# Kernel optimization log

Measured on AMD Instinct MI355X. Metric: run time of the kernel, lower is better.

Reference implementation:

```python
import jax, jax.numpy as jnp
import numpy as np

D_MODEL = 1024
N_HEADS = 16
D_K = D_MODEL // N_HEADS
B, L = 2, 2048


def setup_inputs() -> dict:
    key = jax.random.key(0)
    ks = jax.random.split(key, 11)
    s = 1.0 / np.sqrt(D_MODEL)
    return {
        "q": jax.random.normal(ks[0], (B, L, D_MODEL), jnp.float32),
        "k": jax.random.normal(ks[1], (B, L, D_MODEL), jnp.float32),
        "v": jax.random.normal(ks[2], (B, L, D_MODEL), jnp.float32),
        "w_q": jax.random.normal(ks[3], (D_MODEL, D_MODEL), jnp.float32) * s,
        "b_q": jnp.zeros((D_MODEL,), jnp.float32),
        "w_k": jax.random.normal(ks[4], (D_MODEL, D_MODEL), jnp.float32) * s,
        "b_k": jnp.zeros((D_MODEL,), jnp.float32),
        "w_v": jax.random.normal(ks[5], (D_MODEL, D_MODEL), jnp.float32) * s,
        "b_v": jnp.zeros((D_MODEL,), jnp.float32),
        "w_o": jax.random.normal(ks[6], (D_MODEL, D_MODEL), jnp.float32) * s,
        "b_o": jnp.zeros((D_MODEL,), jnp.float32),
    }


def reference(q, k, v, w_q, b_q, w_k, b_k, w_v, b_v, w_o, b_o):
    b, l, _ = q.shape
    # QKV projections (flax Linear: x @ W + b)
    query = q @ w_q + b_q
    key_ = k @ w_k + b_k
    value = v @ w_v + b_v
    # (B, L, D) -> (B, H, L, d_k)
    query = query.reshape(b, l, N_HEADS, D_K).transpose(0, 2, 1, 3)
    key_ = key_.reshape(b, l, N_HEADS, D_K).transpose(0, 2, 1, 3)
    value = value.reshape(b, l, N_HEADS, D_K).transpose(0, 2, 1, 3)
    # scaled dot-product attention; full (B, H, L, L) score matrix per original
    scores = jnp.einsum("bhqd,bhkd->bhqk", query, key_) / jnp.sqrt(
        jnp.asarray(D_K, query.dtype)
    )
    attn = jax.nn.softmax(scores, axis=-1)
    x = jnp.einsum("bhqk,bhkd->bhqd", attn, value)
    # (B, H, L, d_k) -> (B, L, D)
    x = x.transpose(0, 2, 1, 3).reshape(b, l, D_MODEL)
    return x @ w_o + b_o
```

## Files before the change

### kernel.cpp

```cpp
#include <hip/hip_runtime.h>
#include <hip/hip_bf16.h>


#define D_MODELC 1024
#define N_HEADSC 16
#define D_KC 64
#define BBC 2
#define LLC 2048
#define MMC (BBC * LLC)

typedef __attribute__((ext_vector_type(8))) short v8s;
typedef __attribute__((ext_vector_type(4))) float v4f;

__device__ __forceinline__ float bf2f(unsigned short u) {
    union { unsigned int i; float f; } x;
    x.i = ((unsigned int)u) << 16;
    return x.f;
}
__device__ __forceinline__ unsigned short f2bf(float f) {
    union { float f; unsigned int i; } x;
    x.f = f;
    unsigned int r = x.i + 0x7fffu + ((x.i >> 16) & 1u);
    return (unsigned short)(r >> 16);
}
__device__ __forceinline__ unsigned int pk2bf(float a, float b) {
    __hip_bfloat162 h = __float22bfloat162_rn(make_float2(a, b));
    return *(unsigned int*)&h;
}

#define AS1 __attribute__((address_space(1)))
#define AS3 __attribute__((address_space(3)))

__global__ __launch_bounds__(256) void wtrans(const float* __restrict__ w0,
                                              const float* __restrict__ w1,
                                              const float* __restrict__ w2,
                                              const float* __restrict__ w3,
                                              unsigned short* __restrict__ out) {
    __shared__ unsigned short T[64][65];
    const int z = blockIdx.z;
    const float* W = z == 0 ? w0 : (z == 1 ? w1 : (z == 2 ? w2 : w3));
    unsigned short* O = out + (size_t)z * D_MODELC * D_MODELC;
    const int k0 = blockIdx.y * 64, n0 = blockIdx.x * 64;
    const int c = threadIdx.x & 63, r4 = threadIdx.x >> 6;
#pragma unroll
    for (int i = 0; i < 16; i++) {
        int r = i * 4 + r4;
        T[r][c] = f2bf(W[(size_t)(k0 + r) * D_MODELC + n0 + c]);
    }
    __syncthreads();
#pragma unroll
    for (int i = 0; i < 16; i++) {
        int r = i * 4 + r4;
        O[(size_t)(n0 + r) * D_MODELC + k0 + c] = T[c][r];
    }
}

__global__ __launch_bounds__(256) void vtrans(const unsigned short* __restrict__ Vp,
                                              unsigned short* __restrict__ Vt) {
    __shared__ __align__(16) unsigned short T[64][68];
    const int bh = blockIdx.y;
    const int b = bh >> 4, h = bh & 15;
    const int j0 = blockIdx.x * 64;
    const int t = threadIdx.x;
#pragma unroll
    for (int i = 0; i < 2; i++) {
        int c = i * 256 + t;
        int row = c >> 3, ch = c & 7;
        *(v8s*)&T[row][ch * 8] =
            *(const v8s*)&Vp[((size_t)(b * LLC + j0 + row)) * D_MODELC + h * 64 + ch * 8];
    }
    __syncthreads();
#pragma unroll
    for (int i = 0; i < 2; i++) {
        int c = i * 256 + t;
        int drow = c >> 3, jch = c & 7;
        v8s pk;
#pragma unroll
        for (int u = 0; u < 8; u++) pk[u] = (short)T[jch * 8 + u][drow];
        *(v8s*)&Vt[((size_t)bh * 64 + drow) * LLC + j0 + jch * 8] = pk;
    }
}

template <int MT, int SEGS, bool A_F32, bool OUT_F32>
__global__ __launch_bounds__(256) void gemm_tile(
    const void* __restrict__ A0, const void* __restrict__ A1, const void* __restrict__ A2,
    const unsigned short* __restrict__ Wt,
    const float* __restrict__ bias0, const float* __restrict__ bias1,
    const float* __restrict__ bias2,
    void* __restrict__ C0, void* __restrict__ C1, void* __restrict__ C2,
    float scale0, float scale1, float scale2) {
    const int K = D_MODELC, N = D_MODELC;
    constexpr int MI = MT / 32;
    constexpr int MB = MMC / MT;
    constexpr int PER = SEGS * MB / 8;
    __shared__ __align__(16) unsigned short As[MT * 64];
    __shared__ __align__(16) unsigned short Bs[128 * 64];

    const int t = threadIdx.x;
    const int w = t >> 6, lane = t & 63;
    const int quad = lane >> 4, m15 = lane & 15;
    const int wr = w >> 1, wc = w & 1;
    const int sw = m15 & 7;

    const int flat = blockIdx.x;
    const int xcd = flat & 7;
    const int slot0 = flat >> 3;
    const int group = xcd * PER + (slot0 >> 3);
    const int nb = slot0 & 7;
    const int seg = group / MB;
    const int mb = group % MB;
    const int n0 = nb * 128;
    const int m0 = mb * MT;

    const void* Ap = seg == 0 ? A0 : (seg == 1 ? A1 : A2);
    const unsigned short* Wp = Wt + (size_t)seg * D_MODELC * D_MODELC;
    const float* bias = seg == 0 ? bias0 : (seg == 1 ? bias1 : bias2);
    void* Cp = seg == 0 ? C0 : (seg == 1 ? C1 : C2);
    const float scl = seg == 0 ? scale0 : (seg == 1 ? scale1 : scale2);

    v4f acc[MI][4];
#pragma unroll
    for (int mi = 0; mi < MI; mi++)
#pragma unroll
        for (int ni = 0; ni < 4; ni++) acc[mi][ni] = (v4f){0.f, 0.f, 0.f, 0.f};

    for (int k0 = 0; k0 < K; k0 += 64) {
#pragma unroll
        for (int i = 0; i < 4; i++) {
            int c = i * 256 + t;
            int row = c >> 3, slot = c & 7;
            int j = slot ^ (row & 7);
            const unsigned short* g = Wp + (size_t)(n0 + row) * K + k0 + j * 8;
            __builtin_amdgcn_global_load_lds(
                (const AS1 unsigned int*)g,
                (AS3 unsigned int*)(Bs + (size_t)c * 8), 16, 0, 0);
        }
        if (A_F32) {
#pragma unroll
            for (int i = 0; i < MT / 32; i++) {
                int c = i * 256 + t;
                int row = c >> 3, slot = c & 7;
                int j = slot ^ (row & 7);
                const float* src = (const float*)Ap + (size_t)(m0 + row) * K + k0 + j * 8;
                float4 f0 = ((const float4*)src)[0];
                float4 f1 = ((const float4*)src)[1];
                uint4 pk;
                pk.x = pk2bf(f0.x, f0.y);
                pk.y = pk2bf(f0.z, f0.w);
                pk.z = pk2bf(f1.x, f1.y);
                pk.w = pk2bf(f1.z, f1.w);
                *(uint4*)&As[(size_t)c * 8] = pk;
            }
        } else {
#pragma unroll
            for (int i = 0; i < MT / 32; i++) {
                int c = i * 256 + t;
                int row = c >> 3, slot = c & 7;
                int j = slot ^ (row & 7);
                const unsigned short* g =
                    (const unsigned short*)Ap + (size_t)(m0 + row) * K + k0 + j * 8;
                __builtin_amdgcn_global_load_lds(
                    (const AS1 unsigned int*)g,
                    (AS3 unsigned int*)(As + (size_t)c * 8), 16, 0, 0);
            }
        }
        __syncthreads();

#pragma unroll
        for (int kk = 0; kk < 2; kk++) {
            v8s a[MI], bfr[4];
#pragma unroll
            for (int mi = 0; mi < MI; mi++)
                a[mi] = *(const v8s*)&As[(wr * (MT / 2) + mi * 16 + m15) * 64 +
                                         (((kk * 4 + quad) ^ sw) * 8)];
#pragma unroll
            for (int ni = 0; ni < 4; ni++)
                bfr[ni] = *(const v8s*)&Bs[(wc * 64 + ni * 16 + m15) * 64 +
                                           (((kk * 4 + quad) ^ sw) * 8)];
#pragma unroll
            for (int mi = 0; mi < MI; mi++)
#pragma unroll
                for (int ni = 0; ni < 4; ni++)
                    acc[mi][ni] = __builtin_amdgcn_mfma_f32_16x16x32_bf16(
                        a[mi], bfr[ni], acc[mi][ni], 0, 0, 0);
        }
        __syncthreads();
    }

#pragma unroll
    for (int ni = 0; ni < 4; ni++) {
        int col = n0 + wc * 64 + ni * 16 + m15;
        float bv = bias[col];
#pragma unroll
        for (int mi = 0; mi < MI; mi++) {
#pragma unroll
            for (int r = 0; r < 4; r++) {
                int row = m0 + wr * (MT / 2) + mi * 16 + quad * 4 + r;
                float v = (acc[mi][ni][r] + bv) * scl;
                if (OUT_F32)
                    ((float*)Cp)[(size_t)row * N + col] = v;
                else
                    ((unsigned short*)Cp)[(size_t)row * N + col] = f2bf(v);
            }
        }
    }
}

__global__ __launch_bounds__(512) void attn_mfma(const unsigned short* __restrict__ Qp,
                                                 const unsigned short* __restrict__ Kp,
                                                 const unsigned short* __restrict__ Vt,
                                                 unsigned short* __restrict__ X) {
    __shared__ __align__(16) unsigned short lds[8192 + 8192 + 128 * 72];
    unsigned short* Kb = lds;
    unsigned short* Vb = lds + 8192;
    unsigned short* PQ = lds + 16384;

    const int t = threadIdx.x;
    const int w = t >> 6, lane = t & 63;
    const int quad = lane >> 4, m15 = lane & 15;
    const int bh = blockIdx.y;
    const int b = bh >> 4, h = bh & 15;
    const int q0 = blockIdx.x * 128;
    const size_t hd = (size_t)h * 64;
    const int sw = m15 & 7;

#pragma unroll
    for (int i = 0; i < 2; i++) {
        int chunk = i * 512 + t;
        int row = chunk >> 3, slot = chunk & 7;
        int j = slot ^ (row & 7);
        const unsigned short* g =
            Qp + ((size_t)(b * LLC + q0 + row)) * D_MODELC + hd + j * 8;
        __builtin_amdgcn_global_load_lds((const AS1 unsigned int*)g,
                                         (AS3 unsigned int*)(PQ + (i * 512 + w * 64) * 8),
                                         16, 0, 0);
    }
    {
        int row = t >> 3, slot = t & 7;
        int j = slot ^ (row & 7);
        int gr = 4 * (row & 15) + (row >> 4);
        const unsigned short* gk =
            Kp + ((size_t)(b * LLC + 0 + gr)) * D_MODELC + hd + j * 8;
        __builtin_amdgcn_global_load_lds((const AS1 unsigned int*)gk,
                                         (AS3 unsigned int*)(Kb + (w * 64) * 8), 16, 0, 0);
        const unsigned short* gv = Vt + ((size_t)(bh * 64 + row)) * LLC + 0 + j * 8;
        __builtin_amdgcn_global_load_lds((const AS1 unsigned int*)gv,
                                         (AS3 unsigned int*)(Vb + (w * 64) * 8), 16, 0, 0);
    }
    __syncthreads();

    v8s qa[2];
#pragma unroll
    for (int kk = 0; kk < 2; kk++)
        qa[kk] = *(const v8s*)&PQ[(w * 16 + m15) * 64 + (((kk * 4 + quad) ^ sw) * 8)];
    __syncthreads();

    v8s ones;
#pragma unroll
    for (int u = 0; u < 8; u++) ones[u] = (short)0x3F80;

    v4f O[4];
#pragma unroll
    for (int db = 0; db < 4; db++) O[db] = (v4f){0.f, 0.f, 0.f, 0.f};
    v4f lacc = (v4f){0.f, 0.f, 0.f, 0.f};

    for (int it = 0; it < 32; it++) {
        const int cur = it & 1;
        unsigned short* Kc = Kb + cur * 4096;
        unsigned short* Vc = Vb + cur * 4096;
        if (it < 31) {
            unsigned short* Kn = Kb + (cur ^ 1) * 4096;
            unsigned short* Vn = Vb + (cur ^ 1) * 4096;
            const int k0n = (it + 1) * 64;
            int row = t >> 3, slot = t & 7;
            int j = slot ^ (row & 7);
            int gr = 4 * (row & 15) + (row >> 4);
            const unsigned short* gk =
                Kp + ((size_t)(b * LLC + k0n + gr)) * D_MODELC + hd + j * 8;
            __builtin_amdgcn_global_load_lds((const AS1 unsigned int*)gk,
                                             (AS3 unsigned int*)(Kn + (w * 64) * 8), 16, 0, 0);
            const unsigned short* gv = Vt + ((size_t)(bh * 64 + row)) * LLC + k0n + j * 8;
            __builtin_amdgcn_global_load_lds((const AS1 unsigned int*)gv,
                                             (AS3 unsigned int*)(Vn + (w * 64) * 8), 16, 0, 0);
        }

        v4f S[4];
#pragma unroll
        for (int ns = 0; ns < 4; ns++) S[ns] = (v4f){0.f, 0.f, 0.f, 0.f};
#pragma unroll
        for (int kk = 0; kk < 2; kk++) {
#pragma unroll
            for (int ns = 0; ns < 4; ns++) {
                v8s kf = *(const v8s*)&Kc[(ns * 16 + m15) * 64 +
                                          (((kk * 4 + quad) ^ sw) * 8)];
                S[ns] = __builtin_amdgcn_mfma_f32_16x16x32_bf16(qa[kk], kf, S[ns], 0, 0, 0);
            }
        }

#pragma unroll
        for (int r = 0; r < 4; r++) {
            int prow = w * 16 + quad * 4 + r;
            float e0 = __builtin_amdgcn_exp2f(S[0][r]);
            float e1 = __builtin_amdgcn_exp2f(S[1][r]);
            float e2 = __builtin_amdgcn_exp2f(S[2][r]);
            float e3 = __builtin_amdgcn_exp2f(S[3][r]);
            uint2 pk;
            pk.x = pk2bf(e0, e1);
            pk.y = pk2bf(e2, e3);
            *(uint2*)&PQ[prow * 72 + 4 * m15] = pk;
        }

#pragma unroll
        for (int kk = 0; kk < 2; kk++) {
            v8s a0 = *(const v8s*)&PQ[(w * 16 + m15) * 72 + kk * 32 + quad * 8];
            lacc = __builtin_amdgcn_mfma_f32_16x16x32_bf16(a0, ones, lacc, 0, 0, 0);
#pragma unroll
            for (int db = 0; db < 4; db++) {
                v8s vf = *(const v8s*)&Vc[(db * 16 + m15) * 64 +
                                          (((kk * 4 + quad) ^ sw) * 8)];
                O[db] = __builtin_amdgcn_mfma_f32_16x16x32_bf16(a0, vf, O[db], 0, 0, 0);
            }
        }
        __syncthreads();
    }

#pragma unroll
    for (int r = 0; r < 4; r++) {
        float inv = 1.f / lacc[r];
        int row = q0 + w * 16 + quad * 4 + r;
#pragma unroll
        for (int db = 0; db < 4; db++) {
            X[((size_t)(b * LLC + row)) * D_MODELC + hd + db * 16 + m15] =
                f2bf(O[db][r] * inv);
        }
    }
}

extern "C" void kernel_launch(void* const* d_in, const int* in_sizes, int n_in,
                              void* d_out, int out_size, void* d_ws, size_t ws_size,
                              hipStream_t stream) {
    const float* q = (const float*)d_in[0];
    const float* k = (const float*)d_in[1];
    const float* v = (const float*)d_in[2];
    const float* w_q = (const float*)d_in[3];
    const float* b_q = (const float*)d_in[4];
    const float* w_k = (const float*)d_in[5];
    const float* b_k = (const float*)d_in[6];
    const float* w_v = (const float*)d_in[7];
    const float* b_v = (const float*)d_in[8];
    const float* w_o = (const float*)d_in[9];
    const float* b_o = (const float*)d_in[10];

    const size_t elems = (size_t)MMC * D_MODELC;
    unsigned short* Qp = (unsigned short*)d_ws;
    unsigned short* Kp = Qp + elems;
    unsigned short* Vp = Kp + elems;
    unsigned short* Wt = Vp + elems;
    unsigned short* X = Qp;
    unsigned short* Vt = (unsigned short*)d_out;

    const float QSCALE = 0.125f * 1.44269504088896340736f;

    wtrans<<<dim3(16, 16, 4), 256, 0, stream>>>(w_q, w_k, w_v, w_o, Wt);

    gemm_tile<64, 3, true, false><<<1536, 256, 0, stream>>>(
        q, k, v, Wt, b_q, b_k, b_v, Qp, Kp, Vp, QSCALE, 1.f, 1.f);

    vtrans<<<dim3(LLC / 64, BBC * N_HEADSC), 256, 0, stream>>>(Vp, Vt);

    attn_mfma<<<dim3(LLC / 128, BBC * N_HEADSC), 512, 0, stream>>>(Qp, Kp, Vt, X);

    gemm_tile<32, 1, false, true><<<1024, 256, 0, stream>>>(
        X, X, X, Wt + (size_t)3 * D_MODELC * D_MODELC, b_o, b_o, b_o,
        d_out, d_out, d_out, 1.f, 1.f, 1.f);
}
```

Measured before the change: 227.7 us.

## Double-buffer GEMM LDS tiles and prefetch next K-tile during MFMA compute

```diff
diff --git a/kernel.cpp b/kernel.cpp
--- a/kernel.cpp
+++ b/kernel.cpp
@@ -30,6 +30,8 @@
 
 #define AS1 __attribute__((address_space(1)))
 #define AS3 __attribute__((address_space(3)))
+
+#define CFENCE asm volatile("" ::: "memory")
 
 __global__ __launch_bounds__(256) void wtrans(const float* __restrict__ w0,
                                               const float* __restrict__ w1,
@@ -93,8 +95,10 @@
     constexpr int MI = MT / 32;
     constexpr int MB = MMC / MT;
     constexpr int PER = SEGS * MB / 8;
-    __shared__ __align__(16) unsigned short As[MT * 64];
-    __shared__ __align__(16) unsigned short Bs[128 * 64];
+    constexpr int NT = D_MODELC / 64;
+    constexpr int VC = A_F32 ? (MI * 2 + 4) : (MI + 4);
+    __shared__ __align__(16) unsigned short As[2][MT * 64];
+    __shared__ __align__(16) unsigned short Bs[2][128 * 64];
 
     const int t = threadIdx.x;
     const int w = t >> 6, lane = t & 63;
@@ -118,13 +122,9 @@
     void* Cp = seg == 0 ? C0 : (seg == 1 ? C1 : C2);
     const float scl = seg == 0 ? scale0 : (seg == 1 ? scale1 : scale2);
 
-    v4f acc[MI][4];
-#pragma unroll
-    for (int mi = 0; mi < MI; mi++)
-#pragma unroll
-        for (int ni = 0; ni < 4; ni++) acc[mi][ni] = (v4f){0.f, 0.f, 0.f, 0.f};
-
-    for (int k0 = 0; k0 < K; k0 += 64) {
+    float4 af[MI][2];
+
+    auto stageB = [&](int buf, int k0) {
 #pragma unroll
         for (int i = 0; i < 4; i++) {
             int c = i * 256 + t;
@@ -133,50 +133,64 @@
             const unsigned short* g = Wp + (size_t)(n0 + row) * K + k0 + j * 8;
             __builtin_amdgcn_global_load_lds(
                 (const AS1 unsigned int*)g,
-                (AS3 unsigned int*)(Bs + (size_t)c * 8), 16, 0, 0);
-        }
-        if (A_F32) {
-#pragma unroll
-            for (int i = 0; i < MT / 32; i++) {
-                int c = i * 256 + t;
-                int row = c >> 3, slot = c & 7;
-                int j = slot ^ (row & 7);
-                const float* src = (const float*)Ap + (size_t)(m0 + row) * K + k0 + j * 8;
-                float4 f0 = ((const float4*)src)[0];
-                float4 f1 = ((const float4*)src)[1];
-                uint4 pk;
-                pk.x = pk2bf(f0.x, f0.y);
-                pk.y = pk2bf(f0.z, f0.w);
-                pk.z = pk2bf(f1.x, f1.y);
-                pk.w = pk2bf(f1.z, f1.w);
-                *(uint4*)&As[(size_t)c * 8] = pk;
-            }
-        } else {
-#pragma unroll
-            for (int i = 0; i < MT / 32; i++) {
-                int c = i * 256 + t;
-                int row = c >> 3, slot = c & 7;
-                int j = slot ^ (row & 7);
-                const unsigned short* g =
-                    (const unsigned short*)Ap + (size_t)(m0 + row) * K + k0 + j * 8;
-                __builtin_amdgcn_global_load_lds(
-                    (const AS1 unsigned int*)g,
-                    (AS3 unsigned int*)(As + (size_t)c * 8), 16, 0, 0);
-            }
-        }
-        __syncthreads();
-
+                (AS3 unsigned int*)(&Bs[buf][0] + (size_t)c * 8), 16, 0, 0);
+        }
+    };
+    auto stageA_lds = [&](int buf, int k0) {
+#pragma unroll
+        for (int i = 0; i < MI; i++) {
+            int c = i * 256 + t;
+            int row = c >> 3, slot = c & 7;
+            int j = slot ^ (row & 7);
+            const unsigned short* g =
+                (const unsigned short*)Ap + (size_t)(m0 + row) * K + k0 + j * 8;
+            __builtin_amdgcn_global_load_lds(
+                (const AS1 unsigned int*)g,
+                (AS3 unsigned int*)(&As[buf][0] + (size_t)c * 8), 16, 0, 0);
+        }
+    };
+    auto loadA = [&](int k0) {
+#pragma unroll
+        for (int i = 0; i < MI; i++) {
+            int c = i * 256 + t;
+            int row = c >> 3, slot = c & 7;
+            int j = slot ^ (row & 7);
+            const float* src = (const float*)Ap + (size_t)(m0 + row) * K + k0 + j * 8;
+            af[i][0] = ((const float4*)src)[0];
+            af[i][1] = ((const float4*)src)[1];
+        }
+    };
+    auto writeA = [&](int buf) {
+#pragma unroll
+        for (int i = 0; i < MI; i++) {
+            int c = i * 256 + t;
+            uint4 pk;
+            pk.x = pk2bf(af[i][0].x, af[i][0].y);
+            pk.y = pk2bf(af[i][0].z, af[i][0].w);
+            pk.z = pk2bf(af[i][1].x, af[i][1].y);
+            pk.w = pk2bf(af[i][1].z, af[i][1].w);
+            *(uint4*)&As[buf][(size_t)c * 8] = pk;
+        }
+    };
+
+    v4f acc[MI][4];
+#pragma unroll
+    for (int mi = 0; mi < MI; mi++)
+#pragma unroll
+        for (int ni = 0; ni < 4; ni++) acc[mi][ni] = (v4f){0.f, 0.f, 0.f, 0.f};
+
+    auto compute = [&](int buf) {
 #pragma unroll
         for (int kk = 0; kk < 2; kk++) {
             v8s a[MI], bfr[4];
 #pragma unroll
             for (int mi = 0; mi < MI; mi++)
-                a[mi] = *(const v8s*)&As[(wr * (MT / 2) + mi * 16 + m15) * 64 +
-                                         (((kk * 4 + quad) ^ sw) * 8)];
+                a[mi] = *(const v8s*)&As[buf][(wr * (MT / 2) + mi * 16 + m15) * 64 +
+                                             (((kk * 4 + quad) ^ sw) * 8)];
 #pragma unroll
             for (int ni = 0; ni < 4; ni++)
-                bfr[ni] = *(const v8s*)&Bs[(wc * 64 + ni * 16 + m15) * 64 +
-                                           (((kk * 4 + quad) ^ sw) * 8)];
+                bfr[ni] = *(const v8s*)&Bs[buf][(wc * 64 + ni * 16 + m15) * 64 +
+                                               (((kk * 4 + quad) ^ sw) * 8)];
 #pragma unroll
             for (int mi = 0; mi < MI; mi++)
 #pragma unroll
@@ -184,8 +198,44 @@
                     acc[mi][ni] = __builtin_amdgcn_mfma_f32_16x16x32_bf16(
                         a[mi], bfr[ni], acc[mi][ni], 0, 0, 0);
         }
-        __syncthreads();
-    }
+    };
+
+    if constexpr (A_F32) {
+        loadA(0);
+        stageB(0, 0);
+        writeA(0);
+    } else {
+        stageA_lds(0, 0);
+        stageB(0, 0);
+    }
+
+    int cur = 0;
+#pragma unroll 1
+    for (int it = 0; it < NT - 1; ++it) {
+        const int nxt = cur ^ 1;
+        const int k1 = (it + 1) * 64;
+        if constexpr (A_F32) loadA(k1);
+        else stageA_lds(nxt, k1);
+        stageB(nxt, k1);
+        if constexpr (VC == 8) asm volatile("s_waitcnt vmcnt(8)" ::: "memory");
+        else if constexpr (VC == 6) asm volatile("s_waitcnt vmcnt(6)" ::: "memory");
+        else if constexpr (VC == 5) asm volatile("s_waitcnt vmcnt(5)" ::: "memory");
+        else asm volatile("s_waitcnt vmcnt(0)" ::: "memory");
+        asm volatile("s_waitcnt lgkmcnt(0)" ::: "memory");
+        __builtin_amdgcn_s_barrier();
+        CFENCE;
+        compute(cur);
+        CFENCE;
+        __builtin_amdgcn_s_barrier();
+        CFENCE;
+        if constexpr (A_F32) writeA(nxt);
+        cur = nxt;
+    }
+    asm volatile("s_waitcnt vmcnt(0)" ::: "memory");
+    asm volatile("s_waitcnt lgkmcnt(0)" ::: "memory");
+    __builtin_amdgcn_s_barrier();
+    CFENCE;
+    compute(cur);
 
 #pragma unroll
     for (int ni = 0; ni < 4; ni++) {
```

Result: no change. 230.7 us (+1.3%).
